# Kernel optimization log

Hardware: AMD Instinct MI355X
Metric: run time of the kernel (lower is better)

Reference implementation:

```python
import jax, jax.numpy as jnp
import numpy as np

N, E = 10000, 320000
NF, HF = 256, 256  # input_nf/output_nf, hidden_nf
EPS = 1e-8


def setup_inputs() -> dict:
    key = jax.random.key(0)
    ks = jax.random.split(key, 20)
    h = jax.random.normal(ks[0], (N, NF), jnp.float32)
    coord = jax.random.normal(ks[1], (N, 3), jnp.float32)
    edge_index = jax.random.randint(ks[2], (2, E), 0, N, jnp.int32)

    def dense(k, fan_in, fan_out, scale=None):
        s = scale if scale is not None else 1.0 / np.sqrt(fan_in)
        W = jax.random.normal(k, (fan_in, fan_out), jnp.float32) * s
        b = jnp.zeros((fan_out,), jnp.float32)
        return W, b

    We1, be1 = dense(ks[3], 2 * NF + 1, HF)   # edge_mlp layer 1
    We2, be2 = dense(ks[4], HF, HF)           # edge_mlp layer 2
    Wn1, bn1 = dense(ks[5], HF + NF, HF)      # node_mlp layer 1
    Wn2, bn2 = dense(ks[6], HF, NF)           # node_mlp layer 2
    Wc1, bc1 = dense(ks[7], HF, HF)           # coord_mlp layer 1
    Wc2, bc2 = dense(ks[8], HF, 1, scale=0.001)  # coord_mlp final, tiny init (xavier gain=0.001)
    return dict(h=h, coord=coord, edge_index=edge_index,
                We1=We1, be1=be1, We2=We2, be2=be2,
                Wn1=Wn1, bn1=bn1, Wn2=Wn2, bn2=bn2,
                Wc1=Wc1, bc1=bc1, Wc2=Wc2, bc2=bc2)


def _segment_sum(data, seg_ids, num_segments):
    return jax.ops.segment_sum(data, seg_ids, num_segments=num_segments)


def reference(h, coord, edge_index, We1, be1, We2, be2, Wn1, bn1, Wn2, bn2, Wc1, bc1, Wc2, bc2):
    row, col = edge_index[0], edge_index[1]

    # coord2radial
    coord_diff = coord[row] - coord[col]                    # [E, 3]
    radial = jnp.sum(coord_diff ** 2, axis=1, keepdims=True)  # [E, 1]

    # edge model: MLP on [h_i, h_j, ||x_i - x_j||^2]
    edge_in = jnp.concatenate([h[row], h[col], radial], axis=1)  # [E, 2*NF+1]
    e = jax.nn.silu(edge_in @ We1 + be1)
    edge_feat = jax.nn.silu(e @ We2 + be2)                  # [E, HF]

    # coord model: coord_diff * coord_mlp(edge_feat), mean-aggregated
    c = jax.nn.silu(edge_feat @ Wc1 + bc1)
    trans = coord_diff * (c @ Wc2 + bc2)                    # [E, 3]
    agg_c = _segment_sum(trans, row, coord.shape[0])
    count = _segment_sum(jnp.ones_like(trans), row, coord.shape[0])
    coord_out = coord + agg_c / jnp.clip(count, 1.0)

    # node model: sum-aggregate edge features, concat with h, MLP
    agg_h = _segment_sum(edge_feat, row, h.shape[0])        # [N, HF]
    node_in = jnp.concatenate([h, agg_h], axis=1)           # [N, HF+NF]
    n = jax.nn.silu(node_in @ Wn1 + bn1)
    h_out = n @ Wn2 + bn2                                   # [N, NF]

    return h_out, coord_out
```

## Files before the change

### kernel.cpp

```cpp
#include <hip/hip_runtime.h>
#include <hip/hip_bf16.h>

typedef __bf16 bf16;
typedef __attribute__((ext_vector_type(8))) __bf16 bf16x8;
typedef __attribute__((ext_vector_type(4))) float f32x4;

static_assert(sizeof(bf16x8) == 16, "bf16x8 must be 16B");

constexpr int N_NODES = 10000;
constexpr int N_EDGES = 320000;
constexpr int KPAD    = 264;

__device__ __forceinline__ float silu_f(float x) { return x / (1.0f + __expf(-x)); }

__device__ __forceinline__ void mfma_64x64_k256(const bf16* A, const bf16* BT, int b_stride,
                                                int r, int q, f32x4 acc[4][4]) {
  for (int k0 = 0; k0 < 256; k0 += 32) {
    bf16x8 a[4], b[4];
#pragma unroll
    for (int mi = 0; mi < 4; ++mi)
      a[mi] = *(const bf16x8*)(A + (16 * mi + r) * KPAD + k0 + q * 8);
#pragma unroll
    for (int ni = 0; ni < 4; ++ni)
      b[ni] = *(const bf16x8*)(BT + (size_t)(16 * ni + r) * b_stride + k0 + q * 8);
#pragma unroll
    for (int mi = 0; mi < 4; ++mi)
#pragma unroll
      for (int ni = 0; ni < 4; ++ni)
        acc[mi][ni] = __builtin_amdgcn_mfma_f32_16x16x32_bf16(a[mi], b[ni], acc[mi][ni], 0, 0, 0);
  }
}

__global__ __launch_bounds__(256) void prep_kernel(
    const float* __restrict__ h, const float* __restrict__ We1, const float* __restrict__ We2,
    const float* __restrict__ Wn1, const float* __restrict__ Wn2, const float* __restrict__ Wc1,
    bf16* __restrict__ Hb, bf16* __restrict__ We1T, bf16* __restrict__ Wn1T,
    bf16* __restrict__ We2T, bf16* __restrict__ Wn2T, bf16* __restrict__ Wc1T) {
  int bid = blockIdx.x, tid = threadIdx.x;
  if (bid < 10000) { int i = bid * 256 + tid; Hb[i] = (bf16)h[i]; return; }
  int t = (bid - 10000) * 256 + tid;
  if (t < 131072) { int k = t >> 8, j = t & 255; We1T[j * 512 + k] = (bf16)We1[k * 256 + j]; return; }
  t -= 131072;
  if (t < 131072) { int k = t >> 8, j = t & 255; Wn1T[j * 512 + k] = (bf16)Wn1[k * 256 + j]; return; }
  t -= 131072;
  if (t < 65536) { int k = t >> 8, j = t & 255; We2T[j * 256 + k] = (bf16)We2[k * 256 + j]; return; }
  t -= 65536;
  if (t < 65536) { int k = t >> 8, j = t & 255; Wn2T[j * 256 + k] = (bf16)Wn2[k * 256 + j]; return; }
  t -= 65536;
  if (t < 65536) { int k = t >> 8, j = t & 255; Wc1T[j * 256 + k] = (bf16)Wc1[k * 256 + j]; return; }
}

__global__ __launch_bounds__(256) void hist_kernel(const int* __restrict__ eidx, int* __restrict__ hist) {
  int e = blockIdx.x * 256 + threadIdx.x;
  if (e < N_EDGES) atomicAdd(&hist[eidx[e]], 1);
}

__global__ __launch_bounds__(256) void scan_kernel(const int* __restrict__ hist,
                                                   int* __restrict__ base, int* __restrict__ cursor) {
  __shared__ int partial[256];
  int t = threadIdx.x;
  int s = 0;
#pragma unroll 4
  for (int i = 0; i < 40; ++i) { int idx = t * 40 + i; if (idx < N_NODES) s += hist[idx]; }
  partial[t] = s;
  __syncthreads();
  if (t == 0) { int run = 0; for (int i = 0; i < 256; ++i) { int v = partial[i]; partial[i] = run; run += v; } }
  __syncthreads();
  int run = partial[t];
  for (int i = 0; i < 40; ++i) {
    int idx = t * 40 + i;
    if (idx < N_NODES) { base[idx] = run; cursor[idx] = run; run += hist[idx]; }
  }
}

__global__ __launch_bounds__(256) void scatter_kernel(const int* __restrict__ eidx, int* __restrict__ cursor,
                                                      int* __restrict__ rs, int* __restrict__ cs) {
  int e = blockIdx.x * 256 + threadIdx.x;
  if (e < N_EDGES) {
    int r = eidx[e], c = eidx[N_EDGES + e];
    int p = atomicAdd(&cursor[r], 1);
    rs[p] = r; cs[p] = c;
  }
}

__global__ __launch_bounds__(256, 2) void gemm_pq(const bf16* __restrict__ Hb,
                                                  const bf16* __restrict__ We1T,
                                                  bf16* __restrict__ P, bf16* __restrict__ Q) {
  int tid = threadIdx.x, w = tid >> 6, lane = tid & 63, r = lane & 15, q = lane >> 4;
  int m0 = blockIdx.x * 64;
  const bf16* BT = We1T + (blockIdx.y ? 256 : 0) + (size_t)(w * 64) * 512;
  bf16* OUT = blockIdx.y ? Q : P;
  f32x4 acc[4][4];
#pragma unroll
  for (int mi = 0; mi < 4; ++mi)
#pragma unroll
    for (int ni = 0; ni < 4; ++ni) acc[mi][ni] = (f32x4){0.f, 0.f, 0.f, 0.f};

  for (int k0 = 0; k0 < 256; k0 += 32) {
    bf16x8 a[4], b[4];
#pragma unroll
    for (int mi = 0; mi < 4; ++mi) {
      int m = m0 + 16 * mi + r; if (m > N_NODES - 1) m = N_NODES - 1;
      a[mi] = *(const bf16x8*)(Hb + (size_t)m * 256 + k0 + q * 8);
    }
#pragma unroll
    for (int ni = 0; ni < 4; ++ni)
      b[ni] = *(const bf16x8*)(BT + (size_t)(16 * ni + r) * 512 + k0 + q * 8);
#pragma unroll
    for (int mi = 0; mi < 4; ++mi)
#pragma unroll
      for (int ni = 0; ni < 4; ++ni)
        acc[mi][ni] = __builtin_amdgcn_mfma_f32_16x16x32_bf16(a[mi], b[ni], acc[mi][ni], 0, 0, 0);
  }
#pragma unroll
  for (int ni = 0; ni < 4; ++ni) {
    int n = w * 64 + 16 * ni + (lane & 15);
#pragma unroll
    for (int mi = 0; mi < 4; ++mi)
#pragma unroll
      for (int rg = 0; rg < 4; ++rg) {
        int m = m0 + 16 * mi + q * 4 + rg;
        if (m < N_NODES) OUT[(size_t)m * 256 + n] = (bf16)acc[mi][ni][rg];
      }
  }
}

__global__ __launch_bounds__(256, 4) void edge_kernel(
    const float* __restrict__ coord, const int* __restrict__ rs, const int* __restrict__ cs,
    const float* __restrict__ We1, const float* __restrict__ be1,
    const float* __restrict__ be2, const float* __restrict__ bc1,
    const float* __restrict__ Wc2, const float* __restrict__ bc2,
    const bf16* __restrict__ P, const bf16* __restrict__ Q,
    const bf16* __restrict__ We2T, const bf16* __restrict__ Wc1T,
    float* __restrict__ agg_h, float* __restrict__ agg_c) {
  __shared__ __align__(16) bf16 buf[64 * KPAD];
  __shared__ int s_row[64], s_col[64];
  __shared__ float s_rad[64], s_cd[64][3], s_part[64][4], s_scal[64];

  int tid = threadIdx.x;
  int e0 = blockIdx.x * 64;
  int w = tid >> 6, lane = tid & 63, r = lane & 15, q = lane >> 4;

  if (tid < 64) {
    int e = e0 + tid;
    int ri = rs[e], ci = cs[e];
    s_row[tid] = ri; s_col[tid] = ci;
    float dx = coord[3 * ri + 0] - coord[3 * ci + 0];
    float dy = coord[3 * ri + 1] - coord[3 * ci + 1];
    float dz = coord[3 * ri + 2] - coord[3 * ci + 2];
    s_cd[tid][0] = dx; s_cd[tid][1] = dy; s_cd[tid][2] = dz;
    s_rad[tid] = dx * dx + dy * dy + dz * dz;
  }
  __syncthreads();

  {
    int off = (tid & 31) * 8;
    int esub = tid >> 5;
    float wv[8], bv[8];
#pragma unroll
    for (int j = 0; j < 8; ++j) { wv[j] = We1[512 * 256 + off + j]; bv[j] = be1[off + j]; }
#pragma unroll
    for (int p = 0; p < 8; ++p) {
      int e = p * 8 + esub;
      int ri = s_row[e], ci = s_col[e];
      bf16x8 pv = *(const bf16x8*)(P + (size_t)ri * 256 + off);
      bf16x8 qv = *(const bf16x8*)(Q + (size_t)ci * 256 + off);
      float rad = s_rad[e];
      bf16x8 o;
#pragma unroll
      for (int j = 0; j < 8; ++j)
        o[j] = (bf16)silu_f((float)pv[j] + (float)qv[j] + rad * wv[j] + bv[j]);
      *(bf16x8*)(buf + e * KPAD + off) = o;
    }
  }
  __syncthreads();

  {
    f32x4 acc[4][4];
#pragma unroll
    for (int mi = 0; mi < 4; ++mi)
#pragma unroll
      for (int ni = 0; ni < 4; ++ni) acc[mi][ni] = (f32x4){0.f, 0.f, 0.f, 0.f};
    mfma_64x64_k256(buf, We2T + (size_t)(w * 64) * 256, 256, r, q, acc);
    __syncthreads();
#pragma unroll
    for (int ni = 0; ni < 4; ++ni) {
      int n = w * 64 + 16 * ni + r;
      float bv = be2[n];
#pragma unroll
      for (int mi = 0; mi < 4; ++mi)
#pragma unroll
        for (int rg = 0; rg < 4; ++rg) {
          int m = 16 * mi + q * 4 + rg;
          buf[m * KPAD + n] = (bf16)silu_f(acc[mi][ni][rg] + bv);
        }
    }
  }
  __syncthreads();

  {
    float s = 0.f;
    int cur = s_row[0];
#pragma unroll 4
    for (int e = 0; e < 64; ++e) {
      int re = s_row[e];
      if (re != cur) { atomicAdd(&agg_h[(size_t)cur * 256 + tid], s); s = 0.f; cur = re; }
      s += (float)buf[e * KPAD + tid];
    }
    atomicAdd(&agg_h[(size_t)cur * 256 + tid], s);
  }

  {
    f32x4 acc[4][4];
#pragma unroll
    for (int mi = 0; mi < 4; ++mi)
#pragma unroll
      for (int ni = 0; ni < 4; ++ni) acc[mi][ni] = (f32x4){0.f, 0.f, 0.f, 0.f};
    mfma_64x64_k256(buf, Wc1T + (size_t)(w * 64) * 256, 256, r, q, acc);
    __syncthreads();
#pragma unroll
    for (int ni = 0; ni < 4; ++ni) {
      int n = w * 64 + 16 * ni + r;
      float bv = bc1[n];
#pragma unroll
      for (int mi = 0; mi < 4; ++mi)
#pragma unroll
        for (int rg = 0; rg < 4; ++rg) {
          int m = 16 * mi + q * 4 + rg;
          buf[m * KPAD + n] = (bf16)silu_f(acc[mi][ni][rg] + bv);
        }
    }
  }
  __syncthreads();

  {
    int e = tid >> 2, p = tid & 3;
    float s = 0.f;
#pragma unroll
    for (int kk = 0; kk < 64; kk += 8) {
      bf16x8 v = *(const bf16x8*)(buf + e * KPAD + p * 64 + kk);
#pragma unroll
      for (int j = 0; j < 8; ++j) s += (float)v[j] * Wc2[p * 64 + kk + j];
    }
    s_part[e][p] = s;
  }
  __syncthreads();
  if (tid < 64)
    s_scal[tid] = s_part[tid][0] + s_part[tid][1] + s_part[tid][2] + s_part[tid][3] + bc2[0];
  __syncthreads();

  if (tid < 3) {
    float s = 0.f;
    int cur = s_row[0];
    for (int e = 0; e < 64; ++e) {
      int re = s_row[e];
      if (re != cur) { atomicAdd(&agg_c[3 * cur + tid], s); s = 0.f; cur = re; }
      s += s_cd[e][tid] * s_scal[e];
    }
    atomicAdd(&agg_c[3 * cur + tid], s);
  }
}

__global__ __launch_bounds__(256) void post_kernel(
    const float* __restrict__ agg_h, bf16* __restrict__ Ab,
    const float* __restrict__ coord, const float* __restrict__ agg_c,
    const int* __restrict__ hist, float* __restrict__ coord_out) {
  int bid = blockIdx.x, tid = threadIdx.x;
  if (bid < 10000) { int i = bid * 256 + tid; Ab[i] = (bf16)agg_h[i]; return; }
  int t = (bid - 10000) * 256 + tid;
  if (t < 30000) {
    float c = (float)hist[t / 3]; if (c < 1.f) c = 1.f;
    coord_out[t] = coord[t] + agg_c[t] / c;
  }
}

__global__ __launch_bounds__(256, 2) void node_kernel(
    const bf16* __restrict__ Hb, const bf16* __restrict__ Ab,
    const bf16* __restrict__ Wn1T, const bf16* __restrict__ Wn2T,
    const float* __restrict__ bn1, const float* __restrict__ bn2,
    float* __restrict__ h_out) {
  __shared__ __align__(16) bf16 buf[64 * KPAD];
  int tid = threadIdx.x, w = tid >> 6, lane = tid & 63, r = lane & 15, q = lane >> 4;
  int m0 = blockIdx.x * 64;
  f32x4 acc[4][4];
#pragma unroll
  for (int mi = 0; mi < 4; ++mi)
#pragma unroll
    for (int ni = 0; ni < 4; ++ni) acc[mi][ni] = (f32x4){0.f, 0.f, 0.f, 0.f};

  const bf16* BT1 = Wn1T + (size_t)(w * 64) * 512;
  for (int k0 = 0; k0 < 256; k0 += 32) {
    bf16x8 a[4], b[4];
#pragma unroll
    for (int mi = 0; mi < 4; ++mi) {
      int m = m0 + 16 * mi + r; if (m > N_NODES - 1) m = N_NODES - 1;
      a[mi] = *(const bf16x8*)(Hb + (size_t)m * 256 + k0 + q * 8);
    }
#pragma unroll
    for (int ni = 0; ni < 4; ++ni)
      b[ni] = *(const bf16x8*)(BT1 + (size_t)(16 * ni + r) * 512 + k0 + q * 8);
#pragma unroll
    for (int mi = 0; mi < 4; ++mi)
#pragma unroll
      for (int ni = 0; ni < 4; ++ni)
        acc[mi][ni] = __builtin_amdgcn_mfma_f32_16x16x32_bf16(a[mi], b[ni], acc[mi][ni], 0, 0, 0);
  }
  for (int k0 = 0; k0 < 256; k0 += 32) {
    bf16x8 a[4], b[4];
#pragma unroll
    for (int mi = 0; mi < 4; ++mi) {
      int m = m0 + 16 * mi + r; if (m > N_NODES - 1) m = N_NODES - 1;
      a[mi] = *(const bf16x8*)(Ab + (size_t)m * 256 + k0 + q * 8);
    }
#pragma unroll
    for (int ni = 0; ni < 4; ++ni)
      b[ni] = *(const bf16x8*)(BT1 + (size_t)(16 * ni + r) * 512 + 256 + k0 + q * 8);
#pragma unroll
    for (int mi = 0; mi < 4; ++mi)
#pragma unroll
      for (int ni = 0; ni < 4; ++ni)
        acc[mi][ni] = __builtin_amdgcn_mfma_f32_16x16x32_bf16(a[mi], b[ni], acc[mi][ni], 0, 0, 0);
  }
#pragma unroll
  for (int ni = 0; ni < 4; ++ni) {
    int n = w * 64 + 16 * ni + (lane & 15);
    float bv = bn1[n];
#pragma unroll
    for (int mi = 0; mi < 4; ++mi)
#pragma unroll
      for (int rg = 0; rg < 4; ++rg) {
        int m = 16 * mi + q * 4 + rg;
        buf[m * KPAD + n] = (bf16)silu_f(acc[mi][ni][rg] + bv);
      }
  }
  __syncthreads();
#pragma unroll
  for (int mi = 0; mi < 4; ++mi)
#pragma unroll
    for (int ni = 0; ni < 4; ++ni) acc[mi][ni] = (f32x4){0.f, 0.f, 0.f, 0.f};
  mfma_64x64_k256(buf, Wn2T + (size_t)(w * 64) * 256, 256, r, q, acc);
#pragma unroll
  for (int ni = 0; ni < 4; ++ni) {
    int n = w * 64 + 16 * ni + (lane & 15);
    float bv = bn2[n];
#pragma unroll
    for (int mi = 0; mi < 4; ++mi)
#pragma unroll
      for (int rg = 0; rg < 4; ++rg) {
        int m = m0 + 16 * mi + q * 4 + rg;
        if (m < N_NODES) h_out[(size_t)m * 256 + n] = acc[mi][ni][rg] + bv;
      }
  }
}

extern "C" void kernel_launch(void* const* d_in, const int* in_sizes, int n_in,
                              void* d_out, int out_size, void* d_ws, size_t ws_size,
                              hipStream_t stream) {
  const float* h     = (const float*)d_in[0];
  const float* coord = (const float*)d_in[1];
  const int*   eidx  = (const int*)d_in[2];
  const float* We1 = (const float*)d_in[3];
  const float* be1 = (const float*)d_in[4];
  const float* We2 = (const float*)d_in[5];
  const float* be2 = (const float*)d_in[6];
  const float* Wn1 = (const float*)d_in[7];
  const float* bn1 = (const float*)d_in[8];
  const float* Wn2 = (const float*)d_in[9];
  const float* bn2 = (const float*)d_in[10];
  const float* Wc1 = (const float*)d_in[11];
  const float* bc1 = (const float*)d_in[12];
  const float* Wc2 = (const float*)d_in[13];
  const float* bc2 = (const float*)d_in[14];

  char* ws = (char*)d_ws;
  float* agg_h = (float*)(ws + 0);
  float* agg_c = (float*)(ws + 10240000);
  int*   hist  = (int*)  (ws + 10360000);
  int*   base  = (int*)  (ws + 10400000);
  int*   cursor= (int*)  (ws + 10440000);
  int*   rs    = (int*)  (ws + 10480000);
  int*   cs    = (int*)  (ws + 11760000);
  bf16* Hb   = (bf16*)(ws + 13040000);
  bf16* P    = (bf16*)(ws + 18160000);
  bf16* Q    = (bf16*)(ws + 23280000);
  bf16* Ab   = (bf16*)(ws + 28400000);
  bf16* We1T = (bf16*)(ws + 33520000);
  bf16* Wn1T = (bf16*)(ws + 33782144);
  bf16* We2T = (bf16*)(ws + 34044288);
  bf16* Wn2T = (bf16*)(ws + 34175360);
  bf16* Wc1T = (bf16*)(ws + 34306432);

  float* h_out = (float*)d_out;
  float* coord_out = h_out + (size_t)N_NODES * 256;

  hipMemsetAsync(ws, 0, 10400000, stream);
  prep_kernel<<<11792, 256, 0, stream>>>(h, We1, We2, Wn1, Wn2, Wc1,
                                         Hb, We1T, Wn1T, We2T, Wn2T, Wc1T);
  hist_kernel<<<1250, 256, 0, stream>>>(eidx, hist);
  scan_kernel<<<1, 256, 0, stream>>>(hist, base, cursor);
  scatter_kernel<<<1250, 256, 0, stream>>>(eidx, cursor, rs, cs);
  gemm_pq<<<dim3(157, 2), 256, 0, stream>>>(Hb, We1T, P, Q);
  edge_kernel<<<5000, 256, 0, stream>>>(coord, rs, cs, We1, be1, be2, bc1, Wc2, bc2,
                                        P, Q, We2T, Wc1T, agg_h, agg_c);
  post_kernel<<<10118, 256, 0, stream>>>(agg_h, Ab, coord, agg_c, hist, coord_out);
  node_kernel<<<157, 256, 0, stream>>>(Hb, Ab, Wn1T, Wn2T, bn1, bn2, h_out);
}
```

Baseline: 472.7 us.

## Fuse small kernels, transpose MFMA operands for vector stores, precompute segment runs

```diff
diff --git a/kernel.cpp b/kernel.cpp
--- a/kernel.cpp
+++ b/kernel.cpp
@@ -13,16 +13,22 @@
 
 __device__ __forceinline__ float silu_f(float x) { return x / (1.0f + __expf(-x)); }
 
-__device__ __forceinline__ void mfma_64x64_k256(const bf16* A, const bf16* BT, int b_stride,
-                                                int r, int q, f32x4 acc[4][4]) {
+__device__ __forceinline__ unsigned pk_bf16(float lo, float hi) {
+  unsigned a = __float_as_uint(lo) + 0x8000u;
+  unsigned b = __float_as_uint(hi) + 0x8000u;
+  return __builtin_amdgcn_perm(b, a, 0x07060302u);
+}
+
+__device__ __forceinline__ void mfmaT_k256(const bf16* __restrict__ WT, int wstride, int koff,
+                                           const bf16* Albs, int w, int r, int q, f32x4 acc[4][4]) {
   for (int k0 = 0; k0 < 256; k0 += 32) {
     bf16x8 a[4], b[4];
 #pragma unroll
     for (int mi = 0; mi < 4; ++mi)
-      a[mi] = *(const bf16x8*)(A + (16 * mi + r) * KPAD + k0 + q * 8);
+      a[mi] = *(const bf16x8*)(WT + (size_t)(w * 64 + 16 * mi + r) * wstride + koff + k0 + q * 8);
 #pragma unroll
     for (int ni = 0; ni < 4; ++ni)
-      b[ni] = *(const bf16x8*)(BT + (size_t)(16 * ni + r) * b_stride + k0 + q * 8);
+      b[ni] = *(const bf16x8*)(Albs + (16 * ni + r) * KPAD + k0 + q * 8);
 #pragma unroll
     for (int mi = 0; mi < 4; ++mi)
 #pragma unroll
@@ -34,10 +40,17 @@
 __global__ __launch_bounds__(256) void prep_kernel(
     const float* __restrict__ h, const float* __restrict__ We1, const float* __restrict__ We2,
     const float* __restrict__ Wn1, const float* __restrict__ Wn2, const float* __restrict__ Wc1,
+    const int* __restrict__ eidx,
     bf16* __restrict__ Hb, bf16* __restrict__ We1T, bf16* __restrict__ Wn1T,
-    bf16* __restrict__ We2T, bf16* __restrict__ Wn2T, bf16* __restrict__ Wc1T) {
+    bf16* __restrict__ We2T, bf16* __restrict__ Wn2T, bf16* __restrict__ Wc1T,
+    int* __restrict__ hist) {
   int bid = blockIdx.x, tid = threadIdx.x;
   if (bid < 10000) { int i = bid * 256 + tid; Hb[i] = (bf16)h[i]; return; }
+  if (bid >= 11792) {
+    int e = (bid - 11792) * 256 + tid;
+    if (e < N_EDGES) atomicAdd(&hist[eidx[e]], 1);
+    return;
+  }
   int t = (bid - 10000) * 256 + tid;
   if (t < 131072) { int k = t >> 8, j = t & 255; We1T[j * 512 + k] = (bf16)We1[k * 256 + j]; return; }
   t -= 131072;
@@ -50,23 +63,21 @@
   if (t < 65536) { int k = t >> 8, j = t & 255; Wc1T[j * 256 + k] = (bf16)Wc1[k * 256 + j]; return; }
 }
 
-__global__ __launch_bounds__(256) void hist_kernel(const int* __restrict__ eidx, int* __restrict__ hist) {
-  int e = blockIdx.x * 256 + threadIdx.x;
-  if (e < N_EDGES) atomicAdd(&hist[eidx[e]], 1);
-}
-
 __global__ __launch_bounds__(256) void scan_kernel(const int* __restrict__ hist,
                                                    int* __restrict__ base, int* __restrict__ cursor) {
   __shared__ int partial[256];
   int t = threadIdx.x;
   int s = 0;
-#pragma unroll 4
   for (int i = 0; i < 40; ++i) { int idx = t * 40 + i; if (idx < N_NODES) s += hist[idx]; }
   partial[t] = s;
   __syncthreads();
-  if (t == 0) { int run = 0; for (int i = 0; i < 256; ++i) { int v = partial[i]; partial[i] = run; run += v; } }
-  __syncthreads();
-  int run = partial[t];
+  for (int d = 1; d < 256; d <<= 1) {
+    int v = (t >= d) ? partial[t - d] : 0;
+    __syncthreads();
+    partial[t] += v;
+    __syncthreads();
+  }
+  int run = partial[t] - s;
   for (int i = 0; i < 40; ++i) {
     int idx = t * 40 + i;
     if (idx < N_NODES) { base[idx] = run; cursor[idx] = run; run += hist[idx]; }
@@ -85,11 +96,13 @@
 
 __global__ __launch_bounds__(256, 2) void gemm_pq(const bf16* __restrict__ Hb,
                                                   const bf16* __restrict__ We1T,
+                                                  const float* __restrict__ be1,
                                                   bf16* __restrict__ P, bf16* __restrict__ Q) {
   int tid = threadIdx.x, w = tid >> 6, lane = tid & 63, r = lane & 15, q = lane >> 4;
   int m0 = blockIdx.x * 64;
-  const bf16* BT = We1T + (blockIdx.y ? 256 : 0) + (size_t)(w * 64) * 512;
+  int koff = blockIdx.y ? 256 : 0;
   bf16* OUT = blockIdx.y ? Q : P;
+  bool addb = (blockIdx.y == 0);
   f32x4 acc[4][4];
 #pragma unroll
   for (int mi = 0; mi < 4; ++mi)
@@ -99,13 +112,13 @@
   for (int k0 = 0; k0 < 256; k0 += 32) {
     bf16x8 a[4], b[4];
 #pragma unroll
-    for (int mi = 0; mi < 4; ++mi) {
-      int m = m0 + 16 * mi + r; if (m > N_NODES - 1) m = N_NODES - 1;
-      a[mi] = *(const bf16x8*)(Hb + (size_t)m * 256 + k0 + q * 8);
-    }
-#pragma unroll
-    for (int ni = 0; ni < 4; ++ni)
-      b[ni] = *(const bf16x8*)(BT + (size_t)(16 * ni + r) * 512 + k0 + q * 8);
+    for (int mi = 0; mi < 4; ++mi)
+      a[mi] = *(const bf16x8*)(We1T + (size_t)(w * 64 + 16 * mi + r) * 512 + koff + k0 + q * 8);
+#pragma unroll
+    for (int ni = 0; ni < 4; ++ni) {
+      int m = m0 + 16 * ni + r; if (m > N_NODES - 1) m = N_NODES - 1;
+      b[ni] = *(const bf16x8*)(Hb + (size_t)m * 256 + k0 + q * 8);
+    }
 #pragma unroll
     for (int mi = 0; mi < 4; ++mi)
 #pragma unroll
@@ -113,21 +126,25 @@
         acc[mi][ni] = __builtin_amdgcn_mfma_f32_16x16x32_bf16(a[mi], b[ni], acc[mi][ni], 0, 0, 0);
   }
 #pragma unroll
-  for (int ni = 0; ni < 4; ++ni) {
-    int n = w * 64 + 16 * ni + (lane & 15);
-#pragma unroll
-    for (int mi = 0; mi < 4; ++mi)
-#pragma unroll
-      for (int rg = 0; rg < 4; ++rg) {
-        int m = m0 + 16 * mi + q * 4 + rg;
-        if (m < N_NODES) OUT[(size_t)m * 256 + n] = (bf16)acc[mi][ni][rg];
+  for (int mi = 0; mi < 4; ++mi) {
+    int ch = w * 64 + 16 * mi + 4 * q;
+    float4 bv = addb ? *(const float4*)(be1 + ch) : (float4){0.f, 0.f, 0.f, 0.f};
+#pragma unroll
+    for (int ni = 0; ni < 4; ++ni) {
+      int m = m0 + 16 * ni + r;
+      if (m < N_NODES) {
+        uint2 o;
+        o.x = pk_bf16(acc[mi][ni][0] + bv.x, acc[mi][ni][1] + bv.y);
+        o.y = pk_bf16(acc[mi][ni][2] + bv.z, acc[mi][ni][3] + bv.w);
+        *(uint2*)(OUT + (size_t)m * 256 + ch) = o;
       }
+    }
   }
 }
 
 __global__ __launch_bounds__(256, 4) void edge_kernel(
     const float* __restrict__ coord, const int* __restrict__ rs, const int* __restrict__ cs,
-    const float* __restrict__ We1, const float* __restrict__ be1,
+    const float* __restrict__ We1,
     const float* __restrict__ be2, const float* __restrict__ bc1,
     const float* __restrict__ Wc2, const float* __restrict__ bc2,
     const bf16* __restrict__ P, const bf16* __restrict__ Q,
@@ -136,6 +153,8 @@
   __shared__ __align__(16) bf16 buf[64 * KPAD];
   __shared__ int s_row[64], s_col[64];
   __shared__ float s_rad[64], s_cd[64][3], s_part[64][4], s_scal[64];
+  __shared__ int s_rs[65];
+  __shared__ int s_nrun;
 
   int tid = threadIdx.x;
   int e0 = blockIdx.x * 64;
@@ -153,12 +172,19 @@
   }
   __syncthreads();
 
+  if (tid < 64) {
+    bool bnd = (tid == 0) || (s_row[tid] != s_row[tid - 1]);
+    unsigned long long m = __ballot(bnd);
+    int rank = __popcll(m & ((1ull << tid) - 1ull));
+    if (bnd) s_rs[rank] = tid;
+    if (tid == 0) { int R = __popcll(m); s_nrun = R; s_rs[R] = 64; }
+  }
+
   {
     int off = (tid & 31) * 8;
     int esub = tid >> 5;
-    float wv[8], bv[8];
-#pragma unroll
-    for (int j = 0; j < 8; ++j) { wv[j] = We1[512 * 256 + off + j]; bv[j] = be1[off + j]; }
+    float4 wa = *(const float4*)(We1 + 512 * 256 + off);
+    float4 wb = *(const float4*)(We1 + 512 * 256 + off + 4);
 #pragma unroll
     for (int p = 0; p < 8; ++p) {
       int e = p * 8 + esub;
@@ -166,11 +192,18 @@
       bf16x8 pv = *(const bf16x8*)(P + (size_t)ri * 256 + off);
       bf16x8 qv = *(const bf16x8*)(Q + (size_t)ci * 256 + off);
       float rad = s_rad[e];
-      bf16x8 o;
-#pragma unroll
-      for (int j = 0; j < 8; ++j)
-        o[j] = (bf16)silu_f((float)pv[j] + (float)qv[j] + rad * wv[j] + bv[j]);
-      *(bf16x8*)(buf + e * KPAD + off) = o;
+      float f0 = silu_f((float)pv[0] + (float)qv[0] + rad * wa.x);
+      float f1 = silu_f((float)pv[1] + (float)qv[1] + rad * wa.y);
+      float f2 = silu_f((float)pv[2] + (float)qv[2] + rad * wa.z);
+      float f3 = silu_f((float)pv[3] + (float)qv[3] + rad * wa.w);
+      float f4 = silu_f((float)pv[4] + (float)qv[4] + rad * wb.x);
+      float f5 = silu_f((float)pv[5] + (float)qv[5] + rad * wb.y);
+      float f6 = silu_f((float)pv[6] + (float)qv[6] + rad * wb.z);
+      float f7 = silu_f((float)pv[7] + (float)qv[7] + rad * wb.w);
+      uint4 o;
+      o.x = pk_bf16(f0, f1); o.y = pk_bf16(f2, f3);
+      o.z = pk_bf16(f4, f5); o.w = pk_bf16(f6, f7);
+      *(uint4*)(buf + e * KPAD + off) = o;
     }
   }
   __syncthreads();
@@ -181,54 +214,57 @@
     for (int mi = 0; mi < 4; ++mi)
 #pragma unroll
       for (int ni = 0; ni < 4; ++ni) acc[mi][ni] = (f32x4){0.f, 0.f, 0.f, 0.f};
-    mfma_64x64_k256(buf, We2T + (size_t)(w * 64) * 256, 256, r, q, acc);
+    mfmaT_k256(We2T, 256, 0, buf, w, r, q, acc);
     __syncthreads();
 #pragma unroll
-    for (int ni = 0; ni < 4; ++ni) {
-      int n = w * 64 + 16 * ni + r;
-      float bv = be2[n];
-#pragma unroll
-      for (int mi = 0; mi < 4; ++mi)
-#pragma unroll
-        for (int rg = 0; rg < 4; ++rg) {
-          int m = 16 * mi + q * 4 + rg;
-          buf[m * KPAD + n] = (bf16)silu_f(acc[mi][ni][rg] + bv);
-        }
-    }
-  }
-  __syncthreads();
+    for (int mi = 0; mi < 4; ++mi) {
+      int ch = w * 64 + 16 * mi + 4 * q;
+      float4 bv = *(const float4*)(be2 + ch);
+#pragma unroll
+      for (int ni = 0; ni < 4; ++ni) {
+        int edge = 16 * ni + r;
+        float f0 = silu_f(acc[mi][ni][0] + bv.x);
+        float f1 = silu_f(acc[mi][ni][1] + bv.y);
+        float f2 = silu_f(acc[mi][ni][2] + bv.z);
+        float f3 = silu_f(acc[mi][ni][3] + bv.w);
+        uint2 o; o.x = pk_bf16(f0, f1); o.y = pk_bf16(f2, f3);
+        *(uint2*)(buf + edge * KPAD + ch) = o;
+      }
+    }
+  }
+  __syncthreads();
+
+  f32x4 acc2[4][4];
+#pragma unroll
+  for (int mi = 0; mi < 4; ++mi)
+#pragma unroll
+    for (int ni = 0; ni < 4; ++ni) acc2[mi][ni] = (f32x4){0.f, 0.f, 0.f, 0.f};
+  mfmaT_k256(Wc1T, 256, 0, buf, w, r, q, acc2);
 
   {
-    float s = 0.f;
-    int cur = s_row[0];
-#pragma unroll 4
-    for (int e = 0; e < 64; ++e) {
-      int re = s_row[e];
-      if (re != cur) { atomicAdd(&agg_h[(size_t)cur * 256 + tid], s); s = 0.f; cur = re; }
-      s += (float)buf[e * KPAD + tid];
-    }
-    atomicAdd(&agg_h[(size_t)cur * 256 + tid], s);
-  }
-
-  {
-    f32x4 acc[4][4];
-#pragma unroll
-    for (int mi = 0; mi < 4; ++mi)
-#pragma unroll
-      for (int ni = 0; ni < 4; ++ni) acc[mi][ni] = (f32x4){0.f, 0.f, 0.f, 0.f};
-    mfma_64x64_k256(buf, Wc1T + (size_t)(w * 64) * 256, 256, r, q, acc);
-    __syncthreads();
-#pragma unroll
-    for (int ni = 0; ni < 4; ++ni) {
-      int n = w * 64 + 16 * ni + r;
-      float bv = bc1[n];
-#pragma unroll
-      for (int mi = 0; mi < 4; ++mi)
-#pragma unroll
-        for (int rg = 0; rg < 4; ++rg) {
-          int m = 16 * mi + q * 4 + rg;
-          buf[m * KPAD + n] = (bf16)silu_f(acc[mi][ni][rg] + bv);
-        }
+    int R = s_nrun;
+    for (int rr = 0; rr < R; ++rr) {
+      int st = s_rs[rr], en = s_rs[rr + 1];
+      float s = 0.f;
+      for (int e = st; e < en; ++e) s += (float)buf[e * KPAD + tid];
+      atomicAdd(&agg_h[(size_t)s_row[st] * 256 + tid], s);
+    }
+  }
+  __syncthreads();
+
+#pragma unroll
+  for (int mi = 0; mi < 4; ++mi) {
+    int ch = w * 64 + 16 * mi + 4 * q;
+    float4 bv = *(const float4*)(bc1 + ch);
+#pragma unroll
+    for (int ni = 0; ni < 4; ++ni) {
+      int edge = 16 * ni + r;
+      float f0 = silu_f(acc2[mi][ni][0] + bv.x);
+      float f1 = silu_f(acc2[mi][ni][1] + bv.y);
+      float f2 = silu_f(acc2[mi][ni][2] + bv.z);
+      float f3 = silu_f(acc2[mi][ni][3] + bv.w);
+      uint2 o; o.x = pk_bf16(f0, f1); o.y = pk_bf16(f2, f3);
+      *(uint2*)(buf + edge * KPAD + ch) = o;
     }
   }
   __syncthreads();
@@ -239,8 +275,10 @@
 #pragma unroll
     for (int kk = 0; kk < 64; kk += 8) {
       bf16x8 v = *(const bf16x8*)(buf + e * KPAD + p * 64 + kk);
-#pragma unroll
-      for (int j = 0; j < 8; ++j) s += (float)v[j] * Wc2[p * 64 + kk + j];
+      float4 w0 = *(const float4*)(Wc2 + p * 64 + kk);
+      float4 w1 = *(const float4*)(Wc2 + p * 64 + kk + 4);
+      s += (float)v[0] * w0.x + (float)v[1] * w0.y + (float)v[2] * w0.z + (float)v[3] * w0.w
+         + (float)v[4] * w1.x + (float)v[5] * w1.y + (float)v[6] * w1.z + (float)v[7] * w1.w;
     }
     s_part[e][p] = s;
   }
@@ -250,55 +288,51 @@
   __syncthreads();
 
   if (tid < 3) {
-    float s = 0.f;
-    int cur = s_row[0];
-    for (int e = 0; e < 64; ++e) {
-      int re = s_row[e];
-      if (re != cur) { atomicAdd(&agg_c[3 * cur + tid], s); s = 0.f; cur = re; }
-      s += s_cd[e][tid] * s_scal[e];
-    }
-    atomicAdd(&agg_c[3 * cur + tid], s);
-  }
-}
-
-__global__ __launch_bounds__(256) void post_kernel(
-    const float* __restrict__ agg_h, bf16* __restrict__ Ab,
-    const float* __restrict__ coord, const float* __restrict__ agg_c,
-    const int* __restrict__ hist, float* __restrict__ coord_out) {
-  int bid = blockIdx.x, tid = threadIdx.x;
-  if (bid < 10000) { int i = bid * 256 + tid; Ab[i] = (bf16)agg_h[i]; return; }
-  int t = (bid - 10000) * 256 + tid;
-  if (t < 30000) {
-    float c = (float)hist[t / 3]; if (c < 1.f) c = 1.f;
-    coord_out[t] = coord[t] + agg_c[t] / c;
+    int R = s_nrun;
+    for (int rr = 0; rr < R; ++rr) {
+      int st = s_rs[rr], en = s_rs[rr + 1];
+      float s = 0.f;
+      for (int e = st; e < en; ++e) s += s_cd[e][tid] * s_scal[e];
+      atomicAdd(&agg_c[3 * s_row[st] + tid], s);
+    }
   }
 }
 
 __global__ __launch_bounds__(256, 2) void node_kernel(
-    const bf16* __restrict__ Hb, const bf16* __restrict__ Ab,
+    const bf16* __restrict__ Hb, const float* __restrict__ agg_h,
+    const int* __restrict__ hist, const float* __restrict__ coord, const float* __restrict__ agg_c,
     const bf16* __restrict__ Wn1T, const bf16* __restrict__ Wn2T,
     const float* __restrict__ bn1, const float* __restrict__ bn2,
-    float* __restrict__ h_out) {
+    float* __restrict__ h_out, float* __restrict__ coord_out) {
   __shared__ __align__(16) bf16 buf[64 * KPAD];
   int tid = threadIdx.x, w = tid >> 6, lane = tid & 63, r = lane & 15, q = lane >> 4;
   int m0 = blockIdx.x * 64;
+
+  if (tid < 64) {
+    int m = m0 + tid;
+    if (m < N_NODES) {
+      float c = (float)hist[m]; if (c < 1.f) c = 1.f;
+      coord_out[3 * m + 0] = coord[3 * m + 0] + agg_c[3 * m + 0] / c;
+      coord_out[3 * m + 1] = coord[3 * m + 1] + agg_c[3 * m + 1] / c;
+      coord_out[3 * m + 2] = coord[3 * m + 2] + agg_c[3 * m + 2] / c;
+    }
+  }
+
   f32x4 acc[4][4];
 #pragma unroll
   for (int mi = 0; mi < 4; ++mi)
 #pragma unroll
     for (int ni = 0; ni < 4; ++ni) acc[mi][ni] = (f32x4){0.f, 0.f, 0.f, 0.f};
-
-  const bf16* BT1 = Wn1T + (size_t)(w * 64) * 512;
   for (int k0 = 0; k0 < 256; k0 += 32) {
     bf16x8 a[4], b[4];
 #pragma unroll
-    for (int mi = 0; mi < 4; ++mi) {
-      int m = m0 + 16 * mi + r; if (m > N_NODES - 1) m = N_NODES - 1;
-      a[mi] = *(const bf16x8*)(Hb + (size_t)m * 256 + k0 + q * 8);
-    }
-#pragma unroll
-    for (int ni = 0; ni < 4; ++ni)
-      b[ni] = *(const bf16x8*)(BT1 + (size_t)(16 * ni + r) * 512 + k0 + q * 8);
+    for (int mi = 0; mi < 4; ++mi)
+      a[mi] = *(const bf16x8*)(Wn1T + (size_t)(w * 64 + 16 * mi + r) * 512 + k0 + q * 8);
+#pragma unroll
+    for (int ni = 0; ni < 4; ++ni) {
+      int m = m0 + 16 * ni + r; if (m > N_NODES - 1) m = N_NODES - 1;
+      b[ni] = *(const bf16x8*)(Hb + (size_t)m * 256 + k0 + q * 8);
+    }
 #pragma unroll
     for (int mi = 0; mi < 4; ++mi)
 #pragma unroll
@@ -308,48 +342,64 @@
   for (int k0 = 0; k0 < 256; k0 += 32) {
     bf16x8 a[4], b[4];
 #pragma unroll
-    for (int mi = 0; mi < 4; ++mi) {
-      int m = m0 + 16 * mi + r; if (m > N_NODES - 1) m = N_NODES - 1;
-      a[mi] = *(const bf16x8*)(Ab + (size_t)m * 256 + k0 + q * 8);
-    }
-#pragma unroll
-    for (int ni = 0; ni < 4; ++ni)
-      b[ni] = *(const bf16x8*)(BT1 + (size_t)(16 * ni + r) * 512 + 256 + k0 + q * 8);
+    for (int mi = 0; mi < 4; ++mi)
+      a[mi] = *(const bf16x8*)(Wn1T + (size_t)(w * 64 + 16 * mi + r) * 512 + 256 + k0 + q * 8);
+#pragma unroll
+    for (int ni = 0; ni < 4; ++ni) {
+      int m = m0 + 16 * ni + r; if (m > N_NODES - 1) m = N_NODES - 1;
+      const float* ap = agg_h + (size_t)m * 256 + k0 + q * 8;
+      float4 u = *(const float4*)ap;
+      float4 v = *(const float4*)(ap + 4);
+      uint4 o;
+      o.x = pk_bf16(u.x, u.y); o.y = pk_bf16(u.z, u.w);
+      o.z = pk_bf16(v.x, v.y); o.w = pk_bf16(v.z, v.w);
+      b[ni] = *(const bf16x8*)&o;
+    }
 #pragma unroll
     for (int mi = 0; mi < 4; ++mi)
 #pragma unroll
       for (int ni = 0; ni < 4; ++ni)
         acc[mi][ni] = __builtin_amdgcn_mfma_f32_16x16x32_bf16(a[mi], b[ni], acc[mi][ni], 0, 0, 0);
   }
-#pragma unroll
-  for (int ni = 0; ni < 4; ++ni) {
-    int n = w * 64 + 16 * ni + (lane & 15);
-    float bv = bn1[n];
-#pragma unroll
-    for (int mi = 0; mi < 4; ++mi)
-#pragma unroll
-      for (int rg = 0; rg < 4; ++rg) {
-        int m = 16 * mi + q * 4 + rg;
-        buf[m * KPAD + n] = (bf16)silu_f(acc[mi][ni][rg] + bv);
+  __syncthreads();
+#pragma unroll
+  for (int mi = 0; mi < 4; ++mi) {
+    int ch = w * 64 + 16 * mi + 4 * q;
+    float4 bv = *(const float4*)(bn1 + ch);
+#pragma unroll
+    for (int ni = 0; ni < 4; ++ni) {
+      int lm = 16 * ni + r;
+      float f0 = silu_f(acc[mi][ni][0] + bv.x);
+      float f1 = silu_f(acc[mi][ni][1] + bv.y);
+      float f2 = silu_f(acc[mi][ni][2] + bv.z);
+      float f3 = silu_f(acc[mi][ni][3] + bv.w);
+      uint2 o; o.x = pk_bf16(f0, f1); o.y = pk_bf16(f2, f3);
+      *(uint2*)(buf + lm * KPAD + ch) = o;
+    }
+  }
+  __syncthreads();
+  f32x4 acc2[4][4];
+#pragma unroll
+  for (int mi = 0; mi < 4; ++mi)
+#pragma unroll
+    for (int ni = 0; ni < 4; ++ni) acc2[mi][ni] = (f32x4){0.f, 0.f, 0.f, 0.f};
+  mfmaT_k256(Wn2T, 256, 0, buf, w, r, q, acc2);
+#pragma unroll
+  for (int mi = 0; mi < 4; ++mi) {
+    int ch = w * 64 + 16 * mi + 4 * q;
+    float4 bv = *(const float4*)(bn2 + ch);
+#pragma unroll
+    for (int ni = 0; ni < 4; ++ni) {
+      int m = m0 + 16 * ni + r;
+      if (m < N_NODES) {
+        float4 o;
+        o.x = acc2[mi][ni][0] + bv.x;
+        o.y = acc2[mi][ni][1] + bv.y;
+        o.z = acc2[mi][ni][2] + bv.z;
+        o.w = acc2[mi][ni][3] + bv.w;
+        *(float4*)(h_out + (size_t)m * 256 + ch) = o;
       }
-  }
-  __syncthreads();
-#pragma unroll
-  for (int mi = 0; mi < 4; ++mi)
-#pragma unroll
-    for (int ni = 0; ni < 4; ++ni) acc[mi][ni] = (f32x4){0.f, 0.f, 0.f, 0.f};
-  mfma_64x64_k256(buf, Wn2T + (size_t)(w * 64) * 256, 256, r, q, acc);
-#pragma unroll
-  for (int ni = 0; ni < 4; ++ni) {
-    int n = w * 64 + 16 * ni + (lane & 15);
-    float bv = bn2[n];
-#pragma unroll
-    for (int mi = 0; mi < 4; ++mi)
-#pragma unroll
-      for (int rg = 0; rg < 4; ++rg) {
-        int m = m0 + 16 * mi + q * 4 + rg;
-        if (m < N_NODES) h_out[(size_t)m * 256 + n] = acc[mi][ni][rg] + bv;
-      }
+    }
   }
 }
 
@@ -383,25 +433,23 @@
   bf16* Hb   = (bf16*)(ws + 13040000);
   bf16* P    = (bf16*)(ws + 18160000);
   bf16* Q    = (bf16*)(ws + 23280000);
-  bf16* Ab   = (bf16*)(ws + 28400000);
-  bf16* We1T = (bf16*)(ws + 33520000);
-  bf16* Wn1T = (bf16*)(ws + 33782144);
-  bf16* We2T = (bf16*)(ws + 34044288);
-  bf16* Wn2T = (bf16*)(ws + 34175360);
-  bf16* Wc1T = (bf16*)(ws + 34306432);
+  bf16* We1T = (bf16*)(ws + 28400000);
+  bf16* Wn1T = (bf16*)(ws + 28662144);
+  bf16* We2T = (bf16*)(ws + 28924288);
+  bf16* Wn2T = (bf16*)(ws + 29055360);
+  bf16* Wc1T = (bf16*)(ws + 29186432);
 
   float* h_out = (float*)d_out;
   float* coord_out = h_out + (size_t)N_NODES * 256;
 
   hipMemsetAsync(ws, 0, 10400000, stream);
-  prep_kernel<<<11792, 256, 0, stream>>>(h, We1, We2, Wn1, Wn2, Wc1,
-                                         Hb, We1T, Wn1T, We2T, Wn2T, Wc1T);
-  hist_kernel<<<1250, 256, 0, stream>>>(eidx, hist);
+  prep_kernel<<<13042, 256, 0, stream>>>(h, We1, We2, Wn1, Wn2, Wc1, eidx,
+                                         Hb, We1T, Wn1T, We2T, Wn2T, Wc1T, hist);
   scan_kernel<<<1, 256, 0, stream>>>(hist, base, cursor);
   scatter_kernel<<<1250, 256, 0, stream>>>(eidx, cursor, rs, cs);
-  gemm_pq<<<dim3(157, 2), 256, 0, stream>>>(Hb, We1T, P, Q);
-  edge_kernel<<<5000, 256, 0, stream>>>(coord, rs, cs, We1, be1, be2, bc1, Wc2, bc2,
+  gemm_pq<<<dim3(157, 2), 256, 0, stream>>>(Hb, We1T, be1, P, Q);
+  edge_kernel<<<5000, 256, 0, stream>>>(coord, rs, cs, We1, be2, bc1, Wc2, bc2,
                                         P, Q, We2T, Wc1T, agg_h, agg_c);
-  post_kernel<<<10118, 256, 0, stream>>>(agg_h, Ab, coord, agg_c, hist, coord_out);
-  node_kernel<<<157, 256, 0, stream>>>(Hb, Ab, Wn1T, Wn2T, bn1, bn2, h_out);
-}
+  node_kernel<<<157, 256, 0, stream>>>(Hb, agg_h, hist, coord, agg_c,
+                                       Wn1T, Wn2T, bn1, bn2, h_out, coord_out);
+}
```

Result: faster. 458.2 us (-3.1%).
